# Optimization experiments

Measured on AMD Instinct MI355X. Metric: run time of the kernel, lower is better.

Reference implementation:

```python
import jax, jax.numpy as jnp
import numpy as np

B, C, L = 32, 512, 4096
H, K = 8, 3            # heads, kernel_size
D = C // H             # head dim
G = 32                 # GroupNorm groups
PAD = (K - 1) // 2
EPS = 1e-5
NEG = -1e30


def setup_inputs() -> dict:
    key = jax.random.key(0)
    ks = jax.random.split(key, 7)
    s = 0.02
    return {
        "x": jax.random.normal(ks[0], (B, C, L), dtype=jnp.float32),
        "gamma": jnp.ones((C,), dtype=jnp.float32),
        "beta": jnp.zeros((C,), dtype=jnp.float32),
        "W_k": jax.random.normal(ks[1], (C, H * D), dtype=jnp.float32) * s,
        "W_v": jax.random.normal(ks[2], (C, H * D), dtype=jnp.float32) * s,
        "W_o": jax.random.normal(ks[3], (H * D, C), dtype=jnp.float32) * s,
        "q": jax.random.normal(ks[4], (H, D), dtype=jnp.float32) * s,     # learned queries (QnA)
        "rpe": jax.random.normal(ks[5], (H, K), dtype=jnp.float32) * s,   # relative-position bias
    }


def _group_norm(x, gamma, beta):
    # x: (B, C, L); normalize over (C//G, L) within each of G groups
    b, c, l = x.shape
    xg = x.reshape(b, G, (c // G) * l)
    mu = jnp.mean(xg, axis=-1, keepdims=True)
    var = jnp.var(xg, axis=-1, keepdims=True)
    xn = ((xg - mu) * jax.lax.rsqrt(var + EPS)).reshape(b, c, l)
    return xn * gamma[None, :, None] + beta[None, :, None]


def reference(x, gamma, beta, W_k, W_v, W_o, q, rpe):
    h = _group_norm(x, gamma, beta)                     # (B, C, L)
    ht = jnp.transpose(h, (0, 2, 1))                    # (B, L, C)
    k = (ht @ W_k).reshape(B, L, H, D)                  # (B, L, H, D)
    v = (ht @ W_v).reshape(B, L, H, D)

    scale = 1.0 / np.sqrt(D).astype(np.float32)
    logits = jnp.einsum('blhd,hd->blh', k, q) * scale   # (B, L, H)

    # sliding windows of size K (zero-padded; -inf logits at boundaries)
    lp = jnp.pad(logits, ((0, 0), (PAD, PAD), (0, 0)), constant_values=NEG)
    lwin = jnp.stack([lp[:, j:j + L] for j in range(K)], axis=2)      # (B, L, K, H)
    lwin = lwin + jnp.transpose(rpe)[None, None]                       # rpe: (H,K)->(K,H)
    attn = jax.nn.softmax(lwin, axis=2)                                # (B, L, K, H)

    vp = jnp.pad(v, ((0, 0), (PAD, PAD), (0, 0), (0, 0)))
    vwin = jnp.stack([vp[:, j:j + L] for j in range(K)], axis=2)       # (B, L, K, H, D)
    o = jnp.einsum('blkh,blkhd->blhd', attn, vwin).reshape(B, L, H * D)

    out = (o @ W_o)                                      # (B, L, C)
    return x + jnp.transpose(out, (0, 2, 1))             # residual, (B, C, L)
```

## Files before the change

### kernel.cpp

```cpp
#include <hip/hip_runtime.h>

#define Bb 32
#define Cc 512
#define Ll 4096
#define Hh 8
#define Dd 64
#define Gg 32
#define BLt (Bb * Ll)
#define NKV 520
#define NKVPAD 640

typedef __attribute__((ext_vector_type(4))) float f32x4;
typedef __attribute__((ext_vector_type(8))) short short8;
typedef __attribute__((ext_vector_type(4))) short s16x4;
typedef __attribute__((ext_vector_type(4))) int int4v;

union U16 { int4v v; short s[8]; };

__device__ __forceinline__ float bf2f(short s) {
    unsigned u = ((unsigned)(unsigned short)s) << 16;
    float f; __builtin_memcpy(&f, &u, 4); return f;
}
__device__ __forceinline__ short f2bf(float f) {
    unsigned u; __builtin_memcpy(&u, &f, 4);
    u = (u + 0x7FFFu + ((u >> 16) & 1u)) >> 16;
    return (short)u;
}

__device__ __forceinline__ int kpack(int k) {
    int blk = k >> 5, r = k & 31;
    return blk * 32 + ((r & 15) >> 2) * 8 + ((r >> 4) << 2) + (r & 3);
}

__device__ __forceinline__ int swz_off(int row, int inner) {
    return row * 128 + (inner ^ ((row & 7) << 4));
}

__device__ __forceinline__ void gload16(const short* g, short* l) {
    __builtin_amdgcn_global_load_lds((const __attribute__((address_space(1))) unsigned int*)g,
                                     (__attribute__((address_space(3))) unsigned int*)l,
                                     16, 0, 0);
}

#define BAR() __builtin_amdgcn_s_barrier()
#define SFENCE() __builtin_amdgcn_sched_barrier(0)

__global__ void k_prep(const float* __restrict__ Wk, const float* __restrict__ Wv,
                       const float* __restrict__ Wo, const float* __restrict__ q,
                       short* __restrict__ Wct, short* __restrict__ Wot, int packWo)
{
    int bid = blockIdx.x, t = threadIdx.x;
    if (bid < NKVPAD) {
        int n = bid;
        if (n < 512) {
            for (int k = t; k < 512; k += 64)
                Wct[n * 512 + kpack(k)] = f2bf(Wv[k * 512 + n]);
        } else if (n < NKV) {
            int h = n - 512;
            for (int k = t; k < 512; k += 64) {
                float acc = 0.f;
                for (int d = 0; d < 64; ++d)
                    acc += Wk[k * 512 + h * 64 + d] * q[h * 64 + d];
                Wct[n * 512 + kpack(k)] = f2bf(acc * 0.125f);
            }
        } else {
            for (int k = t; k < 512; k += 64) Wct[n * 512 + kpack(k)] = 0;
        }
    } else {
        int c = bid - NKVPAD;
        for (int k = t; k < 512; k += 64)
            Wot[c * 512 + (packWo ? kpack(k) : k)] = f2bf(Wo[k * 512 + c]);
    }
}

__global__ void k_stats(const float* __restrict__ x, float* __restrict__ stats)
{
    int bg = blockIdx.x;
    const float* p = x + (size_t)bg * 65536;
    int t = threadIdx.x;
    float s = 0.f, ss = 0.f;
    for (int i = t * 4; i < 65536; i += 1024) {
        f32x4 v = *(const f32x4*)(p + i);
        s  += v[0] + v[1] + v[2] + v[3];
        ss += v[0]*v[0] + v[1]*v[1] + v[2]*v[2] + v[3]*v[3];
    }
    for (int o = 32; o > 0; o >>= 1) { s += __shfl_down(s, o); ss += __shfl_down(ss, o); }
    __shared__ float red[8];
    int lane = t & 63, w = t >> 6;
    if (lane == 0) { red[w] = s; red[4 + w] = ss; }
    __syncthreads();
    if (t == 0) {
        float S  = red[0] + red[1] + red[2] + red[3];
        float SS = red[4] + red[5] + red[6] + red[7];
        float mean = S * (1.0f / 65536.0f);
        float var  = SS * (1.0f / 65536.0f) - mean * mean;
        stats[bg * 2]     = mean;
        stats[bg * 2 + 1] = rsqrtf(var + 1e-5f);
    }
}

__global__ void k_norm_t(const float* __restrict__ x, const float* __restrict__ gamma,
                         const float* __restrict__ beta, const float* __restrict__ stats,
                         short* __restrict__ hT)
{
    __shared__ float tile[64 * 65];
    int b = blockIdx.z, c0 = blockIdx.y * 64, l0 = blockIdx.x * 64;
    int t = threadIdx.x;
    int lq = t & 15, cq = t >> 4;
    #pragma unroll
    for (int p = 0; p < 4; ++p) {
        int cl = cq + p * 16;
        int c = c0 + cl;
        float mean = stats[(b * 32 + (c >> 4)) * 2];
        float rstd = stats[(b * 32 + (c >> 4)) * 2 + 1];
        float a  = rstd * gamma[c];
        float bb = beta[c] - mean * a;
        f32x4 v = *(const f32x4*)(x + ((size_t)b << 21) + ((size_t)c << 12) + l0 + lq * 4);
        #pragma unroll
        for (int j = 0; j < 4; ++j) tile[cl * 65 + lq * 4 + j] = v[j] * a + bb;
    }
    __syncthreads();
    int ll = t >> 2, cq4 = t & 3;
    int bl = b * Ll + l0 + ll;
    short hbuf[16];
    #pragma unroll
    for (int j = 0; j < 16; ++j) hbuf[j] = f2bf(tile[(cq4 * 16 + j) * 65 + ll]);
    short* dst = hT + (size_t)bl * 512 + ((c0 >> 5) + (cq4 >> 1)) * 32 + ((cq4 & 1) << 2);
    #pragma unroll
    for (int jj = 0; jj < 4; ++jj) {
        s16x4 v4 = { hbuf[jj*4+0], hbuf[jj*4+1], hbuf[jj*4+2], hbuf[jj*4+3] };
        *(s16x4*)(dst + jj * 8) = v4;
    }
}


__launch_bounds__(256, 2)
__global__ void k_gemm1f(const short* __restrict__ A, const short* __restrict__ Bw,
                         short* __restrict__ vbuf, short* __restrict__ lbuf)
{
    __shared__ short sA[3][8192];
    __shared__ short sB[2][8192];
    const int t = threadIdx.x;
    const int nwg = 1280;
    const int bid = blockIdx.x;
    const int work = (bid & 7) * (nwg >> 3) + (bid >> 3);
    const int n0 = (work % 5) * 128;
    const int mbase = (work / 5) * 512;

    const int lane = t & 63, wid = t >> 6;
    const int wm = wid >> 1, wn = wid & 1;
    const int g = lane >> 4, ln = lane & 15;

    const int srow = wid * 8 + (lane >> 3);
    const int sinner = (((lane & 7) ^ ((lane >> 3) & 7)) << 3);
    const short* gAs = A  + (size_t)(mbase + srow) * 512 + sinner;
    const short* gBs = Bw + (size_t)(n0 + srow) * 512 + sinner;

    f32x4 acc[4][4] = {};

    auto stageA = [&](int s, int buf) {
        size_t off = (size_t)(s >> 3) * 65536 + (size_t)(s & 7) * 64;
        #pragma unroll
        for (int gq = 0; gq < 4; ++gq)
            gload16(gAs + (size_t)gq * 32 * 512 + off, &sA[buf][gq * 2048 + wid * 512]);
    };
    auto stageB = [&](int s, int buf) {
        size_t off = (size_t)(s & 7) * 64;
        #pragma unroll
        for (int gq = 0; gq < 4; ++gq)
            gload16(gBs + (size_t)gq * 32 * 512 + off, &sB[buf][gq * 2048 + wid * 512]);
    };
    auto compute = [&](int ab, int bb) {
        #pragma unroll
        for (int ks = 0; ks < 2; ++ks) {
            short8 af[4], bfr[4];
            #pragma unroll
            for (int i = 0; i < 4; ++i) {
                af[i]  = *(const short8*)((const char*)&sA[ab][0] + swz_off(wm * 64 + i * 16 + ln, ks * 64 + g * 16));
                bfr[i] = *(const short8*)((const char*)&sB[bb][0] + swz_off(wn * 64 + i * 16 + ln, ks * 64 + g * 16));
            }
            #pragma unroll
            for (int mi = 0; mi < 4; ++mi)
                #pragma unroll
                for (int ni = 0; ni < 4; ++ni)
                    acc[mi][ni] = __builtin_amdgcn_mfma_f32_16x16x32_bf16(af[mi], bfr[ni], acc[mi][ni], 0, 0, 0);
        }
    };

    stageB(0, 0); stageB(1, 1); stageA(0, 0); stageA(1, 1); stageA(2, 2);
    #pragma unroll 1
    for (int s = 0; s < 32; ++s) {
        if (s == 31)              asm volatile("s_waitcnt vmcnt(0)"  ::: "memory");
        else if (s == 0 || s == 30) asm volatile("s_waitcnt vmcnt(8)"  ::: "memory");
        else                      asm volatile("s_waitcnt vmcnt(12)" ::: "memory");
        BAR(); SFENCE();
        compute(s % 3, s & 1);
        SFENCE();
        if ((s & 7) == 7) {
            BAR();
            int m0 = mbase + (s >> 3) * 128;
            if (n0 < 512) {
                short* scrW = &sB[s & 1][0] + wid * 2048;
                const int blkq = (lane & 7) >> 2, jq = lane & 3;
                #pragma unroll
                for (int p = 0; p < 2; ++p) {
                    #pragma unroll
                    for (int mh = 0; mh < 2; ++mh)
                        #pragma unroll
                        for (int ni = 0; ni < 4; ++ni)
                            #pragma unroll
                            for (int i = 0; i < 4; ++i)
                                scrW[(mh * 16 + g * 4 + i) * 64 + ni * 16 + ln] = f2bf(acc[p * 2 + mh][ni][i]);
                    asm volatile("s_waitcnt lgkmcnt(0)" ::: "memory"); SFENCE();
                    #pragma unroll
                    for (int it = 0; it < 4; ++it) {
                        int mrl = it * 8 + (lane >> 3);
                        const short* bp = scrW + mrl * 64 + blkq * 32;
                        s16x4 lo = *(const s16x4*)(bp + 4 * jq);
                        s16x4 hi = *(const s16x4*)(bp + 16 + 4 * jq);
                        union { int4v v; s16x4 h[2]; } ov;
                        ov.h[0] = lo; ov.h[1] = hi;
                        int m = m0 + wm * 64 + p * 32 + mrl;
                        int nc = n0 + wn * 64 + blkq * 32 + jq * 8;
                        *(int4v*)(vbuf + (size_t)m * 512 + nc) = ov.v;
                    }
                    asm volatile("s_waitcnt lgkmcnt(0)" ::: "memory"); SFENCE();
                }
            } else {
                if (wn == 0 && ln < 8) {
                    #pragma unroll
                    for (int mi = 0; mi < 4; ++mi)
                        #pragma unroll
                        for (int i = 0; i < 4; ++i) {
                            int m = m0 + wm * 64 + mi * 16 + g * 4 + i;
                            lbuf[(size_t)m * 8 + ln] = f2bf(acc[mi][0][i]);
                        }
                }
            }
            #pragma unroll
            for (int mi = 0; mi < 4; ++mi)
                #pragma unroll
                for (int ni = 0; ni < 4; ++ni)
                    acc[mi][ni] = (f32x4){0.f, 0.f, 0.f, 0.f};
        }
        if (s < 30) {
            BAR();
            stageB(s + 2, s & 1);
            if (s < 29) stageA(s + 3, (s + 3) % 3);
        }
    }
}

__global__ void k_combine(const short* __restrict__ vbuf, const short* __restrict__ lbuf,
                          const float* __restrict__ rpe, short* __restrict__ obuf)
{
    int t = threadIdx.x;
    int bl = blockIdx.x * 16 + (t >> 4);
    int blkd = t & 15;
    int h = blkd >> 1;
    int l = bl & (Ll - 1);
    int bm = (l == 0) ? bl : bl - 1;
    int bp = (l == Ll - 1) ? bl : bl + 1;
    float lg0 = (l > 0)      ? bf2f(lbuf[(size_t)bm * 8 + h]) + rpe[h * 3 + 0] : -1e30f;
    float lg1 =                bf2f(lbuf[(size_t)bl * 8 + h]) + rpe[h * 3 + 1];
    float lg2 = (l < Ll - 1) ? bf2f(lbuf[(size_t)bp * 8 + h]) + rpe[h * 3 + 2] : -1e30f;
    float m = fmaxf(lg1, fmaxf(lg0, lg2));
    float e0 = (l > 0)      ? __expf(lg0 - m) : 0.f;
    float e1 =                __expf(lg1 - m);
    float e2 = (l < Ll - 1) ? __expf(lg2 - m) : 0.f;
    float inv = 1.0f / (e0 + e1 + e2);
    float w0 = e0 * inv, w1 = e1 * inv, w2 = e2 * inv;

    const short8* vm = (const short8*)(vbuf + (size_t)bm * 512 + blkd * 32);
    const short8* v0 = (const short8*)(vbuf + (size_t)bl * 512 + blkd * 32);
    const short8* vp = (const short8*)(vbuf + (size_t)bp * 512 + blkd * 32);
    short8* dst = (short8*)(obuf + (size_t)bl * 512 + blkd * 32);
    #pragma unroll
    for (int qq = 0; qq < 4; ++qq) {
        short8 a = vm[qq], b = v0[qq], c = vp[qq], r;
        #pragma unroll
        for (int j = 0; j < 8; ++j)
            r[j] = f2bf(w0 * bf2f(a[j]) + w1 * bf2f(b[j]) + w2 * bf2f(c[j]));
        dst[qq] = r;
    }
}

__launch_bounds__(256, 2)
__global__ void k_gemm2f(const short* __restrict__ Wot, const short* __restrict__ obuf,
                         const float* __restrict__ x, float* __restrict__ out)
{
    __shared__ short sA[2][8192];
    __shared__ short sB[3][8192];
    const int t = threadIdx.x;
    const int nwg = 1024;
    const int bid = blockIdx.x;
    const int work = (bid & 7) * (nwg >> 3) + (bid >> 3);
    const int n0 = work * 128;

    const int lane = t & 63, wid = t >> 6;
    const int wm = wid >> 1, wn = wid & 1;
    const int g = lane >> 4, ln = lane & 15;

    const int srow = wid * 8 + (lane >> 3);
    const int sinner = (((lane & 7) ^ ((lane >> 3) & 7)) << 3);
    const short* gAs = Wot  + (size_t)srow * 512 + sinner;
    const short* gBs = obuf + (size_t)(n0 + srow) * 512 + sinner;

    f32x4 acc[4][4] = {};

    auto stageA = [&](int s, int buf) {
        size_t off = (size_t)(s >> 3) * 65536 + (size_t)(s & 7) * 64;
        #pragma unroll
        for (int gq = 0; gq < 4; ++gq)
            gload16(gAs + (size_t)gq * 32 * 512 + off, &sA[buf][gq * 2048 + wid * 512]);
    };
    auto stageB = [&](int s, int buf) {
        size_t off = (size_t)(s & 7) * 64;
        #pragma unroll
        for (int gq = 0; gq < 4; ++gq)
            gload16(gBs + (size_t)gq * 32 * 512 + off, &sB[buf][gq * 2048 + wid * 512]);
    };
    auto compute = [&](int ab, int bb) {
        #pragma unroll
        for (int ks = 0; ks < 2; ++ks) {
            short8 af[4], bfr[4];
            #pragma unroll
            for (int i = 0; i < 4; ++i) {
                af[i]  = *(const short8*)((const char*)&sA[ab][0] + swz_off(wm * 64 + i * 16 + ln, ks * 64 + g * 16));
                bfr[i] = *(const short8*)((const char*)&sB[bb][0] + swz_off(wn * 64 + i * 16 + ln, ks * 64 + g * 16));
            }
            #pragma unroll
            for (int mi = 0; mi < 4; ++mi)
                #pragma unroll
                for (int ni = 0; ni < 4; ++ni)
                    acc[mi][ni] = __builtin_amdgcn_mfma_f32_16x16x32_bf16(af[mi], bfr[ni], acc[mi][ni], 0, 0, 0);
        }
    };

    stageA(0, 0); stageA(1, 1); stageB(0, 0); stageB(1, 1); stageB(2, 2);
    #pragma unroll 1
    for (int s = 0; s < 32; ++s) {
        if (s == 31)              asm volatile("s_waitcnt vmcnt(0)"  ::: "memory");
        else if (s == 0 || s == 30) asm volatile("s_waitcnt vmcnt(8)"  ::: "memory");
        else                      asm volatile("s_waitcnt vmcnt(12)" ::: "memory");
        BAR(); SFENCE();
        compute(s & 1, s % 3);
        SFENCE();
        if ((s & 7) == 7) {
            int m0c = (s >> 3) * 128;
            #pragma unroll
            for (int mi = 0; mi < 4; ++mi)
                #pragma unroll
                for (int ni = 0; ni < 4; ++ni)
                    #pragma unroll
                    for (int i = 0; i < 4; ++i) {
                        int c = m0c + wm * 64 + mi * 16 + g * 4 + i;
                        int ng = n0 + wn * 64 + ni * 16 + ln;
                        int b = ng >> 12, l = ng & (Ll - 1);
                        size_t off = ((size_t)b << 21) | ((size_t)c << 12) | (size_t)l;
                        out[off] = x[off] + acc[mi][ni][i];
                    }
            #pragma unroll
            for (int mi = 0; mi < 4; ++mi)
                #pragma unroll
                for (int ni = 0; ni < 4; ++ni)
                    acc[mi][ni] = (f32x4){0.f, 0.f, 0.f, 0.f};
        }
        if (s < 30) {
            BAR();
            stageA(s + 2, s & 1);
            if (s < 29) stageB(s + 3, (s + 3) % 3);
        }
    }
}

__launch_bounds__(256, 2)
__global__ void k_gemm1_fb(const short* __restrict__ A, const short* __restrict__ Bw,
                           short* __restrict__ kv)
{
    __shared__ short sA[2][8192];
    __shared__ short sB[2][8192];
    const int t = threadIdx.x;
    const int m0 = blockIdx.y * 128;
    const int n0 = blockIdx.x * 128;
    const int lane = t & 63, wid = t >> 6;
    const int wm = wid >> 1, wn = wid & 1;
    const int g = lane >> 4, ln = lane & 15;

    const int srow = wid * 8 + (lane >> 3);
    const int sinner = (((lane & 7) ^ ((lane >> 3) & 7)) << 3);
    const short* gAs = A  + (size_t)(m0 + srow) * 512 + sinner;
    const short* gBs = Bw + (size_t)(n0 + srow) * 512 + sinner;

    f32x4 acc[4][4] = {};

    auto stage = [&](int kt, int buf) {
        #pragma unroll
        for (int gq = 0; gq < 4; ++gq) {
            gload16(gAs + (size_t)gq * 32 * 512 + kt * 64, &sA[buf][gq * 2048 + wid * 512]);
            gload16(gBs + (size_t)gq * 32 * 512 + kt * 64, &sB[buf][gq * 2048 + wid * 512]);
        }
    };
    auto compute = [&](int buf) {
        #pragma unroll
        for (int ks = 0; ks < 2; ++ks) {
            short8 af[4], bfr[4];
            #pragma unroll
            for (int i = 0; i < 4; ++i) {
                af[i]  = *(const short8*)((const char*)&sA[buf][0] + swz_off(wm * 64 + i * 16 + ln, ks * 64 + g * 16));
                bfr[i] = *(const short8*)((const char*)&sB[buf][0] + swz_off(wn * 64 + i * 16 + ln, ks * 64 + g * 16));
            }
            #pragma unroll
            for (int mi = 0; mi < 4; ++mi)
                #pragma unroll
                for (int ni = 0; ni < 4; ++ni)
                    acc[mi][ni] = __builtin_amdgcn_mfma_f32_16x16x32_bf16(af[mi], bfr[ni], acc[mi][ni], 0, 0, 0);
        }
    };

    stage(0, 0);
    __syncthreads();
    #pragma unroll 1
    for (int kt = 0; kt < 8; ++kt) {
        if (kt < 7) stage(kt + 1, (kt + 1) & 1);
        compute(kt & 1);
        __syncthreads();
    }

    #pragma unroll
    for (int mi = 0; mi < 4; ++mi)
        #pragma unroll
        for (int ni = 0; ni < 4; ++ni) {
            int n = n0 + wn * 64 + ni * 16 + ln;
            if (n < NKV) {
                #pragma unroll
                for (int i = 0; i < 4; ++i) {
                    int m = m0 + wm * 64 + mi * 16 + g * 4 + i;
                    kv[(size_t)m * NKV + n] = f2bf(acc[mi][ni][i]);
                }
            }
        }
}

__global__ void k_attnw(const short* __restrict__ kv, const float* __restrict__ rpe,
                        float* __restrict__ attnW)
{
    int tid = blockIdx.x * 256 + threadIdx.x;
    int bl = tid >> 3, h = tid & 7;
    int l = bl & (Ll - 1);
    float lg[3];
    #pragma unroll
    for (int j = 0; j < 3; ++j) {
        bool valid = (j == 1) || (j == 0 && l > 0) || (j == 2 && l < Ll - 1);
        lg[j] = valid ? (bf2f(kv[(size_t)(bl + j - 1) * NKV + 512 + h]) + rpe[h * 3 + j])
                      : -1e30f;
    }
    float m = fmaxf(lg[0], fmaxf(lg[1], lg[2]));
    float e0 = __expf(lg[0] - m), e1 = __expf(lg[1] - m), e2 = __expf(lg[2] - m);
    float inv = 1.0f / (e0 + e1 + e2);
    f32x4 w = { e0 * inv, e1 * inv, e2 * inv, 0.0f };
    *(f32x4*)(attnW + (size_t)bl * 32 + h * 4) = w;
}

__launch_bounds__(256, 2)
__global__ void k_gemm2_fused(const short* __restrict__ Wot, const short* __restrict__ kv,
                              const float* __restrict__ attnW, const float* __restrict__ x,
                              float* __restrict__ out)
{
    __shared__ short sA[2][8192];
    __shared__ short sB[2][8192];
    const int t = threadIdx.x;
    const int m0 = blockIdx.x * 128;
    const int n0 = blockIdx.y * 128;
    const int lane = t & 63, wid = t >> 6;
    const int wm = wid >> 1, wn = wid & 1;
    const int g = lane >> 4, ln = lane & 15;
    const int sr = t >> 1, ksh = t & 1;

    const short* gA = Wot + (size_t)(m0 + sr) * 512 + ksh * 32;
    const int nrow = n0 + sr;
    const int lpos = nrow & (Ll - 1);
    const int nm1 = (lpos == 0) ? nrow : nrow - 1;
    const int np1 = (lpos == Ll - 1) ? nrow : nrow + 1;
    const short* gV0 = kv + (size_t)nrow * NKV + ksh * 32;
    const short* gVm = kv + (size_t)nm1  * NKV + ksh * 32;
    const short* gVp = kv + (size_t)np1  * NKV + ksh * 32;
    const float* gW = attnW + (size_t)nrow * 32;

    f32x4 acc[4][4] = {};
    U16 ra[4], rbm[4], rb0[4], rbp[4];
    f32x4 wv;

    auto load_tile = [&](int kt) {
        #pragma unroll
        for (int qq = 0; qq < 4; ++qq) {
            ra[qq].v  = *(const int4v*)(gA  + kt * 64 + qq * 8);
            rbm[qq].v = *(const int4v*)(gVm + kt * 64 + qq * 8);
            rb0[qq].v = *(const int4v*)(gV0 + kt * 64 + qq * 8);
            rbp[qq].v = *(const int4v*)(gVp + kt * 64 + qq * 8);
        }
        wv = *(const f32x4*)(gW + kt * 4);
    };
    auto write_tile = [&](int buf) {
        short ob[32];
        #pragma unroll
        for (int qq = 0; qq < 4; ++qq)
            #pragma unroll
            for (int j = 0; j < 8; ++j) {
                float o = wv[0] * bf2f(rbm[qq].s[j]) + wv[1] * bf2f(rb0[qq].s[j])
                        + wv[2] * bf2f(rbp[qq].s[j]);
                ob[qq * 8 + j] = f2bf(o);
            }
        #pragma unroll
        for (int f = 0; f < 4; ++f) {
            U16 wa, wb;
            #pragma unroll
            for (int j = 0; j < 4; ++j) {
                wa.s[j]     = ra[f >> 1].s[(f & 1) * 4 + j];
                wa.s[4 + j] = ra[2 + (f >> 1)].s[(f & 1) * 4 + j];
                wb.s[j]     = ob[4 * f + j];
                wb.s[4 + j] = ob[16 + 4 * f + j];
            }
            int off = swz_off(sr, ksh * 64 + f * 16);
            *(int4v*)((char*)&sA[buf][0] + off) = wa.v;
            *(int4v*)((char*)&sB[buf][0] + off) = wb.v;
        }
    };
    auto compute = [&](int buf) {
        #pragma unroll
        for (int ks = 0; ks < 2; ++ks) {
            short8 af[4], bfr[4];
            #pragma unroll
            for (int i = 0; i < 4; ++i) {
                af[i]  = *(const short8*)((const char*)&sA[buf][0] + swz_off(wm * 64 + i * 16 + ln, ks * 64 + g * 16));
                bfr[i] = *(const short8*)((const char*)&sB[buf][0] + swz_off(wn * 64 + i * 16 + ln, ks * 64 + g * 16));
            }
            #pragma unroll
            for (int mi = 0; mi < 4; ++mi)
                #pragma unroll
                for (int ni = 0; ni < 4; ++ni)
                    acc[mi][ni] = __builtin_amdgcn_mfma_f32_16x16x32_bf16(af[mi], bfr[ni], acc[mi][ni], 0, 0, 0);
        }
    };

    load_tile(0); write_tile(0); __syncthreads();
    #pragma unroll 1
    for (int kt = 0; kt < 8; ++kt) {
        if (kt < 7) load_tile(kt + 1);
        compute(kt & 1);
        if (kt < 7) write_tile((kt + 1) & 1);
        __syncthreads();
    }

    #pragma unroll
    for (int mi = 0; mi < 4; ++mi)
        #pragma unroll
        for (int ni = 0; ni < 4; ++ni)
            #pragma unroll
            for (int i = 0; i < 4; ++i) {
                int c = m0 + wm * 64 + mi * 16 + g * 4 + i;
                int ng = n0 + wn * 64 + ni * 16 + ln;
                int b = ng >> 12, l = ng & (Ll - 1);
                size_t off = ((size_t)b << 21) | ((size_t)c << 12) | (size_t)l;
                out[off] = x[off] + acc[mi][ni][i];
            }
}

extern "C" void kernel_launch(void* const* d_in, const int* in_sizes, int n_in,
                              void* d_out, int out_size, void* d_ws, size_t ws_size,
                              hipStream_t stream)
{
    const float* x     = (const float*)d_in[0];
    const float* gamma = (const float*)d_in[1];
    const float* beta  = (const float*)d_in[2];
    const float* Wk    = (const float*)d_in[3];
    const float* Wv    = (const float*)d_in[4];
    const float* Wo    = (const float*)d_in[5];
    const float* q     = (const float*)d_in[6];
    const float* rpe   = (const float*)d_in[7];
    float* out = (float*)d_out;
    char* ws = (char*)d_ws;

    const size_t MB128 = 134217728ull;
    const size_t MAIN_WS = MB128 * 2 + 655360 + 524288 + 2097152 + 8192;

    if (ws_size >= MAIN_WS) {
        short* obuf  = (short*)(ws);
        short* vbuf  = (short*)(ws + MB128);
        short* Wct   = (short*)(ws + 2 * MB128);
        short* Wot   = (short*)(ws + 2 * MB128 + 655360);
        short* lbuf  = (short*)(ws + 2 * MB128 + 655360 + 524288);
        float* stats = (float*)(ws + 2 * MB128 + 655360 + 524288 + 2097152);
        short* hT    = (short*)d_out;

        k_prep<<<1152, 64, 0, stream>>>(Wk, Wv, Wo, q, Wct, Wot, 1);
        k_stats<<<1024, 256, 0, stream>>>(x, stats);
        k_norm_t<<<dim3(64, 8, 32), 256, 0, stream>>>(x, gamma, beta, stats, hT);
        k_gemm1f<<<1280, 256, 0, stream>>>(hT, Wct, vbuf, lbuf);
        k_combine<<<8192, 256, 0, stream>>>(vbuf, lbuf, rpe, obuf);
        k_gemm2f<<<1024, 256, 0, stream>>>(Wot, obuf, x, out);
    } else {
        short* Wct   = (short*)(ws + 0);
        short* Wot   = (short*)(ws + 655360);
        float* stats = (float*)(ws + 1179648);
        float* attnW = (float*)(ws + 1187840);
        short* kv    = (short*)(ws + 17965056);
        short* hT    = (short*)d_out;

        k_prep<<<1152, 64, 0, stream>>>(Wk, Wv, Wo, q, Wct, Wot, 0);
        k_stats<<<1024, 256, 0, stream>>>(x, stats);
        k_norm_t<<<dim3(64, 8, 32), 256, 0, stream>>>(x, gamma, beta, stats, hT);
        k_gemm1_fb<<<dim3(5, 1024), 256, 0, stream>>>(hT, Wct, kv);
        k_attnw<<<4096, 256, 0, stream>>>(kv, rpe, attnW);
        k_gemm2_fused<<<dim3(4, 1024), 256, 0, stream>>>(Wot, kv, attnW, x, out);
    }
}
```

Measured before the change: 555.0 us.

## Fold logit column into V GEMM tiles and vectorize residual epilogue via LDS

The first GEMM no longer launches a separate N-tile for the 8 logit columns. Each block keeps the q-projected weight rows in LDS and computes the logits with extra MFMAs alongside its V tile, and only the ntile-0 blocks write them. This cuts the grid from 1280 to 1024 blocks and avoids a mostly-wasted 128-wide tile, at the cost of a 4x redundant logit compute and double rather than triple buffering of A. The second GEMM epilogue now stages accumulators through swizzled LDS so the x reads and out writes are 16-byte vectors instead of scalar strided accesses.

```diff
diff --git a/kernel.cpp b/kernel.cpp
--- a/kernel.cpp
+++ b/kernel.cpp
@@ -138,18 +138,35 @@
 __global__ void k_gemm1f(const short* __restrict__ A, const short* __restrict__ Bw,
                          short* __restrict__ vbuf, short* __restrict__ lbuf)
 {
-    __shared__ short sA[3][8192];
+    __shared__ short sA[2][8192];
     __shared__ short sB[2][8192];
+    __shared__ short wqlds[8192];
     const int t = threadIdx.x;
-    const int nwg = 1280;
+    const int nwg = 1024;
     const int bid = blockIdx.x;
     const int work = (bid & 7) * (nwg >> 3) + (bid >> 3);
-    const int n0 = (work % 5) * 128;
-    const int mbase = (work / 5) * 512;
+    const int ntile = work & 3;
+    const int n0 = ntile * 128;
+    const int mbase = (work >> 2) * 512;
 
     const int lane = t & 63, wid = t >> 6;
     const int wm = wid >> 1, wn = wid & 1;
     const int g = lane >> 4, ln = lane & 15;
+
+    {
+        int row = t >> 5;
+        int cp = (t & 31) * 2;
+        int4v v0 = *(const int4v*)(Bw + (size_t)(512 + row) * 512 + cp * 8);
+        int4v v1 = *(const int4v*)(Bw + (size_t)(512 + row) * 512 + cp * 8 + 8);
+        *(int4v*)((char*)wqlds + row * 1024 + ((cp * 16) ^ ((row & 7) << 4))) = v0;
+        *(int4v*)((char*)wqlds + row * 1024 + (((cp + 1) * 16) ^ ((row & 7) << 4))) = v1;
+        int4v z = {0, 0, 0, 0};
+        int row2 = 8 + (t >> 5);
+        *(int4v*)((char*)wqlds + row2 * 1024 + ((cp * 16) ^ ((row2 & 7) << 4))) = z;
+        *(int4v*)((char*)wqlds + row2 * 1024 + (((cp + 1) * 16) ^ ((row2 & 7) << 4))) = z;
+    }
+    asm volatile("s_waitcnt vmcnt(0) lgkmcnt(0)" ::: "memory");
+    BAR(); SFENCE();
 
     const int srow = wid * 8 + (lane >> 3);
     const int sinner = (((lane & 7) ^ ((lane >> 3) & 7)) << 3);
@@ -157,49 +174,51 @@
     const short* gBs = Bw + (size_t)(n0 + srow) * 512 + sinner;
 
     f32x4 acc[4][4] = {};
-
-    auto stageA = [&](int s, int buf) {
-        size_t off = (size_t)(s >> 3) * 65536 + (size_t)(s & 7) * 64;
-        #pragma unroll
-        for (int gq = 0; gq < 4; ++gq)
-            gload16(gAs + (size_t)gq * 32 * 512 + off, &sA[buf][gq * 2048 + wid * 512]);
-    };
-    auto stageB = [&](int s, int buf) {
-        size_t off = (size_t)(s & 7) * 64;
-        #pragma unroll
-        for (int gq = 0; gq < 4; ++gq)
-            gload16(gBs + (size_t)gq * 32 * 512 + off, &sB[buf][gq * 2048 + wid * 512]);
-    };
-    auto compute = [&](int ab, int bb) {
+    f32x4 accq[4] = {};
+
+    auto stage = [&](int kt, int buf) {
+        size_t offA = (size_t)(kt >> 3) * 65536 + (size_t)(kt & 7) * 64;
+        size_t offB = (size_t)(kt & 7) * 64;
+        #pragma unroll
+        for (int gq = 0; gq < 4; ++gq) {
+            gload16(gAs + (size_t)gq * 32 * 512 + offA, &sA[buf][gq * 2048 + wid * 512]);
+            gload16(gBs + (size_t)gq * 32 * 512 + offB, &sB[buf][gq * 2048 + wid * 512]);
+        }
+    };
+    auto compute = [&](int buf, int kk) {
         #pragma unroll
         for (int ks = 0; ks < 2; ++ks) {
-            short8 af[4], bfr[4];
+            short8 af[4], bfr[4], bq;
             #pragma unroll
             for (int i = 0; i < 4; ++i) {
-                af[i]  = *(const short8*)((const char*)&sA[ab][0] + swz_off(wm * 64 + i * 16 + ln, ks * 64 + g * 16));
-                bfr[i] = *(const short8*)((const char*)&sB[bb][0] + swz_off(wn * 64 + i * 16 + ln, ks * 64 + g * 16));
-            }
+                af[i]  = *(const short8*)((const char*)&sA[buf][0] + swz_off(wm * 64 + i * 16 + ln, ks * 64 + g * 16));
+                bfr[i] = *(const short8*)((const char*)&sB[buf][0] + swz_off(wn * 64 + i * 16 + ln, ks * 64 + g * 16));
+            }
+            bq = *(const short8*)((const char*)wqlds + ln * 1024 +
+                                  ((kk * 128 + ks * 64 + g * 16) ^ ((ln & 7) << 4)));
             #pragma unroll
             for (int mi = 0; mi < 4; ++mi)
                 #pragma unroll
                 for (int ni = 0; ni < 4; ++ni)
                     acc[mi][ni] = __builtin_amdgcn_mfma_f32_16x16x32_bf16(af[mi], bfr[ni], acc[mi][ni], 0, 0, 0);
-        }
-    };
-
-    stageB(0, 0); stageB(1, 1); stageA(0, 0); stageA(1, 1); stageA(2, 2);
+            #pragma unroll
+            for (int mi = 0; mi < 4; ++mi)
+                accq[mi] = __builtin_amdgcn_mfma_f32_16x16x32_bf16(af[mi], bq, accq[mi], 0, 0, 0);
+        }
+    };
+
+    stage(0, 0); stage(1, 1);
     #pragma unroll 1
     for (int s = 0; s < 32; ++s) {
-        if (s == 31)              asm volatile("s_waitcnt vmcnt(0)"  ::: "memory");
-        else if (s == 0 || s == 30) asm volatile("s_waitcnt vmcnt(8)"  ::: "memory");
-        else                      asm volatile("s_waitcnt vmcnt(12)" ::: "memory");
+        if (s < 31) asm volatile("s_waitcnt vmcnt(8)" ::: "memory");
+        else        asm volatile("s_waitcnt vmcnt(0)" ::: "memory");
         BAR(); SFENCE();
-        compute(s % 3, s & 1);
+        compute(s & 1, s & 7);
         SFENCE();
         if ((s & 7) == 7) {
             BAR();
             int m0 = mbase + (s >> 3) * 128;
-            if (n0 < 512) {
+            {
                 short* scrW = &sB[s & 1][0] + wid * 2048;
                 const int blkq = (lane & 7) >> 2, jq = lane & 3;
                 #pragma unroll
@@ -226,28 +245,25 @@
                     }
                     asm volatile("s_waitcnt lgkmcnt(0)" ::: "memory"); SFENCE();
                 }
-            } else {
-                if (wn == 0 && ln < 8) {
+            }
+            if (ntile == 0 && wn == 0 && ln < 8) {
+                #pragma unroll
+                for (int mi = 0; mi < 4; ++mi)
                     #pragma unroll
-                    for (int mi = 0; mi < 4; ++mi)
-                        #pragma unroll
-                        for (int i = 0; i < 4; ++i) {
-                            int m = m0 + wm * 64 + mi * 16 + g * 4 + i;
-                            lbuf[(size_t)m * 8 + ln] = f2bf(acc[mi][0][i]);
-                        }
-                }
-            }
-            #pragma unroll
-            for (int mi = 0; mi < 4; ++mi)
+                    for (int i = 0; i < 4; ++i) {
+                        int m = m0 + wm * 64 + mi * 16 + g * 4 + i;
+                        lbuf[(size_t)m * 8 + ln] = f2bf(accq[mi][i]);
+                    }
+            }
+            #pragma unroll
+            for (int mi = 0; mi < 4; ++mi) {
                 #pragma unroll
                 for (int ni = 0; ni < 4; ++ni)
                     acc[mi][ni] = (f32x4){0.f, 0.f, 0.f, 0.f};
-        }
-        if (s < 30) {
-            BAR();
-            stageB(s + 2, s & 1);
-            if (s < 29) stageA(s + 3, (s + 3) % 3);
-        }
+                accq[mi] = (f32x4){0.f, 0.f, 0.f, 0.f};
+            }
+        }
+        if (s < 30) { BAR(); stage(s + 2, s & 1); }
     }
 }
 
@@ -347,19 +363,35 @@
         compute(s & 1, s % 3);
         SFENCE();
         if ((s & 7) == 7) {
+            BAR();
+            float* scr = (float*)((char*)&sA[s & 1][0] + wid * 4096);
             int m0c = (s >> 3) * 128;
-            #pragma unroll
-            for (int mi = 0; mi < 4; ++mi)
+            const int r4 = lane >> 4, lcm = (lane & 15) * 4;
+            #pragma unroll
+            for (int p = 0; p < 4; ++p) {
                 #pragma unroll
                 for (int ni = 0; ni < 4; ++ni)
                     #pragma unroll
                     for (int i = 0; i < 4; ++i) {
-                        int c = m0c + wm * 64 + mi * 16 + g * 4 + i;
-                        int ng = n0 + wn * 64 + ni * 16 + ln;
-                        int b = ng >> 12, l = ng & (Ll - 1);
-                        size_t off = ((size_t)b << 21) | ((size_t)c << 12) | (size_t)l;
-                        out[off] = x[off] + acc[mi][ni][i];
+                        int r = g * 4 + i;
+                        int col = (ni * 16 + ln) ^ ((((r & 3) ^ (r >> 2)) & 3) << 4);
+                        scr[r * 64 + col] = acc[p][ni][i];
                     }
+                asm volatile("s_waitcnt lgkmcnt(0)" ::: "memory"); SFENCE();
+                #pragma unroll
+                for (int j = 0; j < 4; ++j) {
+                    int rr = r4 + 4 * j;
+                    int cst = lcm ^ ((((rr & 3) ^ (rr >> 2)) & 3) << 4);
+                    f32x4 sv = *(const f32x4*)&scr[rr * 64 + cst];
+                    int c = m0c + wm * 64 + p * 16 + rr;
+                    int ng = n0 + wn * 64 + lcm;
+                    int b = ng >> 12, l = ng & (Ll - 1);
+                    size_t off = ((size_t)b << 21) | ((size_t)c << 12) | (size_t)l;
+                    f32x4 xv = *(const f32x4*)(x + off);
+                    *(f32x4*)(out + off) = xv + sv;
+                }
+                asm volatile("s_waitcnt lgkmcnt(0)" ::: "memory"); SFENCE();
+            }
             #pragma unroll
             for (int mi = 0; mi < 4; ++mi)
                 #pragma unroll
@@ -596,7 +628,7 @@
         k_prep<<<1152, 64, 0, stream>>>(Wk, Wv, Wo, q, Wct, Wot, 1);
         k_stats<<<1024, 256, 0, stream>>>(x, stats);
         k_norm_t<<<dim3(64, 8, 32), 256, 0, stream>>>(x, gamma, beta, stats, hT);
-        k_gemm1f<<<1280, 256, 0, stream>>>(hT, Wct, vbuf, lbuf);
+        k_gemm1f<<<1024, 256, 0, stream>>>(hT, Wct, vbuf, lbuf);
         k_combine<<<8192, 256, 0, stream>>>(vbuf, lbuf, rpe, obuf);
         k_gemm2f<<<1024, 256, 0, stream>>>(Wot, obuf, x, out);
     } else {
```

Result: faster. 535.8 us (-3.5%).
